# Optimization experiments

Hardware: AMD Instinct MI355X
Metric: run time of the kernel (lower is better)

The kernel has to match this reference:

```python
import jax, jax.numpy as jnp
import numpy as np

H = 16          # num heads
DH = 64         # head dim
D = H * DH      # hidden = 1024


def setup_inputs() -> dict:
    key = jax.random.key(0)
    ks = jax.random.split(key, 9)
    s = 1.0 / np.sqrt(D)
    return {
        "hidden_states": jax.random.normal(ks[0], (4, 2048, D), dtype=jnp.float32),
        "Wq": jax.random.normal(ks[1], (D, D), dtype=jnp.float32) * s,
        "bq": jax.random.normal(ks[2], (D,), dtype=jnp.float32) * 0.02,
        "Wk": jax.random.normal(ks[3], (D, D), dtype=jnp.float32) * s,
        "bk": jax.random.normal(ks[4], (D,), dtype=jnp.float32) * 0.02,
        "Wv": jax.random.normal(ks[5], (D, D), dtype=jnp.float32) * s,
        "bv": jax.random.normal(ks[6], (D,), dtype=jnp.float32) * 0.02,
        "Wo": jax.random.normal(ks[7], (D, D), dtype=jnp.float32) * s,
        "bo": jax.random.normal(ks[8], (D,), dtype=jnp.float32) * 0.02,
    }


def _split_heads(x):  # [B,S,D] -> [B,H,S,DH]
    B, S, _ = x.shape
    return x.reshape(B, S, H, DH).transpose(0, 2, 1, 3)


def reference(hidden_states, Wq, bq, Wk, bk, Wv, bv, Wo, bo):
    # torch Linear: y = x @ W.T + b  (W stored as [out, in])
    q = _split_heads(jnp.einsum('bsd,ed->bse', hidden_states, Wq) + bq)
    k = _split_heads(jnp.einsum('bsd,ed->bse', hidden_states, Wk) + bk)
    v = _split_heads(jnp.einsum('bsd,ed->bse', hidden_states, Wv) + bv)
    scores = jnp.einsum('bhqd,bhkd->bhqk', q, k) / np.sqrt(DH)
    probs = jax.nn.softmax(scores, axis=-1)  # fused softmax+matmul in original
    ctx = jnp.einsum('bhqk,bhkd->bhqd', probs, v)
    B, _, S, _ = ctx.shape
    ctx = ctx.transpose(0, 2, 1, 3).reshape(B, S, D)
    out = jnp.einsum('bsd,ed->bse', ctx, Wo) + bo
    return out  # weights are None (vis=False); dropout rate asserted 0
```

## Files before the change

kernel.cpp:

```cpp
#include <hip/hip_runtime.h>


typedef __bf16 bf16;
typedef __bf16 bf16x8 __attribute__((ext_vector_type(8)));
typedef __bf16 bf16x4 __attribute__((ext_vector_type(4)));
typedef short  short4v __attribute__((ext_vector_type(4)));
typedef float  floatx4 __attribute__((ext_vector_type(4)));

#define NB   4
#define SEQ  2048
#define NH   16
#define DH   64
#define DIM  1024
#define MTOT (NB * SEQ)

__device__ __forceinline__ floatx4 zero4() {
    floatx4 z; z[0] = 0.f; z[1] = 0.f; z[2] = 0.f; z[3] = 0.f; return z;
}

__device__ __forceinline__ void load_lds16(const bf16* g, bf16* l) {
    __builtin_amdgcn_global_load_lds(
        (__attribute__((address_space(1))) void*)g,
        (__attribute__((address_space(3))) void*)l,
        16, 0, 0);
}

__device__ __forceinline__ short4v pk4(float a, float b, float c, float d) {
    bf16x4 t; t[0] = (bf16)a; t[1] = (bf16)b; t[2] = (bf16)c; t[3] = (bf16)d;
    return __builtin_bit_cast(short4v, t);
}

__global__ __launch_bounds__(256) void cvt_kernel(const float* __restrict__ in,
                                                  bf16* __restrict__ out, int n) {
    int i = (blockIdx.x * 256 + threadIdx.x) * 4;
    if (i + 3 < n) {
        float4 f = *(const float4*)(in + i);
        bf16x4 o;
        o[0] = (bf16)f.x; o[1] = (bf16)f.y; o[2] = (bf16)f.z; o[3] = (bf16)f.w;
        *(bf16x4*)(out + i) = o;
    }
}

__global__ __launch_bounds__(256) void cvt4_kernel(const float* __restrict__ w0,
                                                   const float* __restrict__ w1,
                                                   const float* __restrict__ w2,
                                                   const float* __restrict__ w3,
                                                   bf16* __restrict__ out) {
    const float* src = (blockIdx.y == 0) ? w0 : (blockIdx.y == 1) ? w1
                     : (blockIdx.y == 2) ? w2 : w3;
    size_t i = ((size_t)blockIdx.x * 256 + threadIdx.x) * 4;
    float4 f = *(const float4*)(src + i);
    bf16x4 o;
    o[0] = (bf16)f.x; o[1] = (bf16)f.y; o[2] = (bf16)f.z; o[3] = (bf16)f.w;
    *(bf16x4*)(out + (size_t)blockIdx.y * (DIM * DIM) + i) = o;
}

__global__ __launch_bounds__(256) void gemm_qkv(const bf16* __restrict__ A,
                                                const bf16* __restrict__ W,
                                                const float* __restrict__ bq,
                                                const float* __restrict__ bk,
                                                const float* __restrict__ bv,
                                                bf16* __restrict__ Qo,
                                                bf16* __restrict__ Ko,
                                                bf16* __restrict__ Vt) {
    __shared__ __align__(16) bf16 As[128 * 32];
    __shared__ __align__(16) bf16 Bs[128 * 32];
    __shared__ __align__(16) bf16 Ts[64 * 136];

    const int tid  = threadIdx.x;
    const int wave = tid >> 6, lane = tid & 63;
    const int quad = lane >> 4, l16 = lane & 15;
    const int sel = blockIdx.x >> 3;
    const int nt  = blockIdx.x & 7;
    const int m0 = blockIdx.y * 128, n0 = nt * 128;
    const int wm = (wave & 1) * 64, wn = (wave >> 1) * 64;
    const bf16* Wsel = W + (size_t)(sel * DIM + n0) * DIM;
    const float* bias = (sel == 0) ? bq : (sel == 1) ? bk : bv;

    floatx4 acc[4][4];
#pragma unroll
    for (int mi = 0; mi < 4; mi++)
#pragma unroll
        for (int ni = 0; ni < 4; ni++) acc[mi][ni] = zero4();

    for (int k0 = 0; k0 < DIM; k0 += 32) {
        __syncthreads();
#pragma unroll
        for (int i = 0; i < 2; i++) {
            const int cb = wave * 128 + i * 64;
            const int c  = cb + lane;
            const int row = c >> 2;
            const int kc  = (c & 3) * 8;
            load_lds16(A + (size_t)(m0 + row) * DIM + k0 + kc, &As[cb * 8]);
            load_lds16(Wsel + (size_t)row * DIM + k0 + kc, &Bs[cb * 8]);
        }
        __syncthreads();

        bf16x8 af[4], bfr[4];
#pragma unroll
        for (int mi = 0; mi < 4; mi++)
            af[mi] = *(const bf16x8*)&As[(wm + mi * 16 + l16) * 32 + quad * 8];
#pragma unroll
        for (int ni = 0; ni < 4; ni++)
            bfr[ni] = *(const bf16x8*)&Bs[(wn + ni * 16 + l16) * 32 + quad * 8];
#pragma unroll
        for (int mi = 0; mi < 4; mi++)
#pragma unroll
            for (int ni = 0; ni < 4; ni++)
                acc[mi][ni] = __builtin_amdgcn_mfma_f32_16x16x32_bf16(
                    af[mi], bfr[ni], acc[mi][ni], 0, 0, 0);
    }

    if (sel < 2) {
        bf16* C = (sel == 0) ? Qo : Ko;
#pragma unroll
        for (int mi = 0; mi < 4; mi++) {
            const int rbase = m0 + wm + mi * 16 + quad * 4;
#pragma unroll
            for (int ni = 0; ni < 4; ni++) {
                const int col = n0 + wn + ni * 16 + l16;
                const float bval = bias[col];
#pragma unroll
                for (int i = 0; i < 4; i++)
                    C[(size_t)(rbase + i) * DIM + col] = (bf16)(acc[mi][ni][i] + bval);
            }
        }
    } else {
        const int b  = blockIdx.y >> 4;
        const int s0 = (blockIdx.y & 15) * 128;
#pragma unroll
        for (int r = 0; r < 2; r++) {
            __syncthreads();
            if ((wave >> 1) == r) {
#pragma unroll
                for (int mi = 0; mi < 4; mi++) {
                    const int m_l = wm + mi * 16 + quad * 4;
#pragma unroll
                    for (int ni = 0; ni < 4; ni++) {
                        const int n_loc = ni * 16 + l16;
                        const float bval = bias[n0 + 64 * r + n_loc];
#pragma unroll
                        for (int i = 0; i < 4; i++)
                            Ts[n_loc * 136 + m_l + i] = (bf16)(acc[mi][ni][i] + bval);
                    }
                }
            }
            __syncthreads();
            const int hh = 2 * nt + r;
            bf16* obase = Vt + ((size_t)(b * NH + hh) * DH) * SEQ + s0;
#pragma unroll
            for (int p = 0; p < 4; p++) {
                const int chunk = p * 256 + tid;
                const int row = chunk >> 4, c0 = (chunk & 15) * 8;
                bf16x8 v = *(const bf16x8*)&Ts[row * 136 + c0];
                *(bf16x8*)(obase + (size_t)row * SEQ + c0) = v;
            }
        }
    }
}

__global__ __launch_bounds__(256) void gemm_out(const bf16* __restrict__ A,
                                                const bf16* __restrict__ W,
                                                const float* __restrict__ bias,
                                                float* __restrict__ C) {
    __shared__ __align__(16) bf16 As[128 * 32];
    __shared__ __align__(16) bf16 Bs[128 * 32];

    const int tid  = threadIdx.x;
    const int wave = tid >> 6, lane = tid & 63;
    const int quad = lane >> 4, l16 = lane & 15;
    const int m0 = blockIdx.y * 128, n0 = blockIdx.x * 128;
    const int wm = (wave & 1) * 64, wn = (wave >> 1) * 64;

    floatx4 acc[4][4];
#pragma unroll
    for (int mi = 0; mi < 4; mi++)
#pragma unroll
        for (int ni = 0; ni < 4; ni++) acc[mi][ni] = zero4();

    for (int k0 = 0; k0 < DIM; k0 += 32) {
        __syncthreads();
#pragma unroll
        for (int i = 0; i < 2; i++) {
            const int cb = wave * 128 + i * 64;
            const int c  = cb + lane;
            const int row = c >> 2;
            const int kc  = (c & 3) * 8;
            load_lds16(A + (size_t)(m0 + row) * DIM + k0 + kc, &As[cb * 8]);
            load_lds16(W + (size_t)(n0 + row) * DIM + k0 + kc, &Bs[cb * 8]);
        }
        __syncthreads();

        bf16x8 af[4], bfr[4];
#pragma unroll
        for (int mi = 0; mi < 4; mi++)
            af[mi] = *(const bf16x8*)&As[(wm + mi * 16 + l16) * 32 + quad * 8];
#pragma unroll
        for (int ni = 0; ni < 4; ni++)
            bfr[ni] = *(const bf16x8*)&Bs[(wn + ni * 16 + l16) * 32 + quad * 8];
#pragma unroll
        for (int mi = 0; mi < 4; mi++)
#pragma unroll
            for (int ni = 0; ni < 4; ni++)
                acc[mi][ni] = __builtin_amdgcn_mfma_f32_16x16x32_bf16(
                    af[mi], bfr[ni], acc[mi][ni], 0, 0, 0);
    }

#pragma unroll
    for (int mi = 0; mi < 4; mi++) {
        const int rbase = m0 + wm + mi * 16 + quad * 4;
#pragma unroll
        for (int ni = 0; ni < 4; ni++) {
            const int col = n0 + wn + ni * 16 + l16;
            const float bval = bias[col];
#pragma unroll
            for (int i = 0; i < 4; i++)
                C[(size_t)(rbase + i) * DIM + col] = acc[mi][ni][i] + bval;
        }
    }
}

__global__ __launch_bounds__(256, 4) void attn_kernel(const bf16* __restrict__ Q,
                                                      const bf16* __restrict__ K,
                                                      const bf16* __restrict__ Vt,
                                                      bf16* __restrict__ Ctx) {
    __shared__ __align__(16) bf16 Ks[64 * 64];
    __shared__ __align__(16) bf16 Vs[64 * 64];

    const int tid  = threadIdx.x;
    const int wave = tid >> 6, lane = tid & 63;
    const int quad = lane >> 4, l16 = lane & 15;
    const int bh = blockIdx.x >> 4;
    const int qb = blockIdx.x & 15;
    const int b  = bh >> 4, h = bh & 15;

    const size_t base_bh = (size_t)b * SEQ * DIM + (size_t)h * DH;
    const size_t base_v  = (size_t)bh * DH * SEQ;
    const bf16* Kg = K + base_bh;
    const bf16* Vg = Vt + base_v;
    const int qt = qb * 128 + wave * 32;

    bf16x8 aq[2][2];
#pragma unroll
    for (int m = 0; m < 2; m++) {
        const bf16* qp = Q + base_bh + (size_t)(qt + m * 16 + l16) * DIM + quad * 8;
        aq[m][0] = *(const bf16x8*)qp;
        aq[m][1] = *(const bf16x8*)(qp + 32);
    }

    const short4v ones4 = pk4(1.f, 1.f, 1.f, 1.f);
    const float CEXP = 0.18033688f;

    floatx4 acc[2][4], accl[2];
#pragma unroll
    for (int m = 0; m < 2; m++) {
        accl[m] = zero4();
#pragma unroll
        for (int dt = 0; dt < 4; dt++) acc[m][dt] = zero4();
    }

    for (int kv0 = 0; kv0 < SEQ; kv0 += 64) {
        __syncthreads();
#pragma unroll
        for (int i = 0; i < 2; i++) {
            const int cb = wave * 128 + i * 64;
            const int c  = cb + lane;
            const int row = c >> 3;
            const int col8 = (c & 7) ^ (row & 7);
            load_lds16(Kg + (size_t)(kv0 + row) * DIM + col8 * 8, &Ks[cb * 8]);
            load_lds16(Vg + (size_t)row * SEQ + kv0 + col8 * 8, &Vs[cb * 8]);
        }
        __syncthreads();

#pragma unroll
        for (int t = 0; t < 4; t++) {
            const int krow = t * 16 + l16;
            const bf16x8 kb0 = *(const bf16x8*)&Ks[(krow * 8 + (quad ^ (krow & 7))) * 8];
            const bf16x8 kb1 = *(const bf16x8*)&Ks[(krow * 8 + ((4 + quad) ^ (krow & 7))) * 8];
            short4v vb[4];
#pragma unroll
            for (int dt = 0; dt < 4; dt++) {
                const int d = dt * 16 + l16;
                vb[dt] = __builtin_bit_cast(short4v, *(const bf16x4*)
                    &Vs[(d * 8 + ((t * 2 + (quad >> 1)) ^ (d & 7))) * 8 + (quad & 1) * 4]);
            }
#pragma unroll
            for (int m = 0; m < 2; m++) {
                floatx4 z = zero4();
                z = __builtin_amdgcn_mfma_f32_16x16x32_bf16(kb0, aq[m][0], z, 0, 0, 0);
                z = __builtin_amdgcn_mfma_f32_16x16x32_bf16(kb1, aq[m][1], z, 0, 0, 0);
                const short4v p = pk4(exp2f(z[0] * CEXP), exp2f(z[1] * CEXP),
                                      exp2f(z[2] * CEXP), exp2f(z[3] * CEXP));
#pragma unroll
                for (int dt = 0; dt < 4; dt++)
                    acc[m][dt] = __builtin_amdgcn_mfma_f32_16x16x16bf16_1k(
                        p, vb[dt], acc[m][dt], 0, 0, 0);
                accl[m] = __builtin_amdgcn_mfma_f32_16x16x16bf16_1k(
                    p, ones4, accl[m], 0, 0, 0);
            }
        }
    }

#pragma unroll
    for (int m = 0; m < 2; m++) {
        float inv[4];
#pragma unroll
        for (int i = 0; i < 4; i++) inv[i] = 1.0f / accl[m][i];
        bf16* cp = Ctx + base_bh + (size_t)(qt + m * 16 + quad * 4) * DIM + l16;
#pragma unroll
        for (int i = 0; i < 4; i++)
#pragma unroll
            for (int dt = 0; dt < 4; dt++)
                cp[(size_t)i * DIM + dt * 16] = (bf16)(acc[m][dt][i] * inv[i]);
    }
}

extern "C" void kernel_launch(void* const* d_in, const int* in_sizes, int n_in,
                              void* d_out, int out_size, void* d_ws, size_t ws_size,
                              hipStream_t stream) {
    const float* X  = (const float*)d_in[0];
    const float* Wq = (const float*)d_in[1];
    const float* bq = (const float*)d_in[2];
    const float* Wk = (const float*)d_in[3];
    const float* bk = (const float*)d_in[4];
    const float* Wv = (const float*)d_in[5];
    const float* bv = (const float*)d_in[6];
    const float* Wo = (const float*)d_in[7];
    const float* bo = (const float*)d_in[8];
    float* out = (float*)d_out;

    const size_t MD = (size_t)MTOT * DIM;
    const size_t DD = (size_t)DIM * DIM;

    bf16* Xb  = (bf16*)d_ws;
    bf16* Qb  = Xb + MD;
    bf16* Kb  = Qb + MD;
    bf16* Vtb = Kb + MD;
    bf16* Wqb = Vtb + MD;
    bf16* Wob = Wqb + 3 * DD;
    if (ws_size < (MD * 4 + DD * 4) * sizeof(bf16)) return;

    cvt_kernel<<<(int)(MD / 4 / 256), 256, 0, stream>>>(X, Xb, (int)MD);
    cvt4_kernel<<<dim3(DIM * DIM / 1024, 4), 256, 0, stream>>>(Wq, Wk, Wv, Wo, Wqb);

    gemm_qkv<<<dim3(24, MTOT / 128), 256, 0, stream>>>(Xb, Wqb, bq, bk, bv,
                                                       Qb, Kb, Vtb);

    attn_kernel<<<NB * NH * (SEQ / 128), 256, 0, stream>>>(Qb, Kb, Vtb, Xb);

    gemm_out<<<dim3(8, MTOT / 128), 256, 0, stream>>>(Xb, Wob, bo, out);
}
```

Baseline: 319.1 us.

## Fold softmax scale into Q projection and halve attention query tile per block

Pre-multiplies Q by the exp2 softmax scale in the QKV GEMM epilogue, removing a multiply per score in attention. Attention blocks now process 64 queries with 16 per wave instead of 128 with 32, doubling the grid and raising the occupancy hint to 6. This cuts registers per thread and improves latency hiding, but halves K/V tile reuse per load, doubling K/V traffic and sync overhead per FLOP.

```diff
diff --git a/kernel.cpp b/kernel.cpp
--- a/kernel.cpp
+++ b/kernel.cpp
@@ -13,6 +13,8 @@
 #define DH   64
 #define DIM  1024
 #define MTOT (NB * SEQ)
+
+#define CEXP 0.18033688f
 
 __device__ __forceinline__ floatx4 zero4() {
     floatx4 z; z[0] = 0.f; z[1] = 0.f; z[2] = 0.f; z[3] = 0.f; return z;
@@ -76,6 +78,7 @@
     const int wm = (wave & 1) * 64, wn = (wave >> 1) * 64;
     const bf16* Wsel = W + (size_t)(sel * DIM + n0) * DIM;
     const float* bias = (sel == 0) ? bq : (sel == 1) ? bk : bv;
+    const float scale = (sel == 0) ? CEXP : 1.0f;
 
     floatx4 acc[4][4];
 #pragma unroll
@@ -122,7 +125,8 @@
                 const float bval = bias[col];
 #pragma unroll
                 for (int i = 0; i < 4; i++)
-                    C[(size_t)(rbase + i) * DIM + col] = (bf16)(acc[mi][ni][i] + bval);
+                    C[(size_t)(rbase + i) * DIM + col] =
+                        (bf16)((acc[mi][ni][i] + bval) * scale);
             }
         }
     } else {
@@ -220,7 +224,7 @@
     }
 }
 
-__global__ __launch_bounds__(256, 4) void attn_kernel(const bf16* __restrict__ Q,
+__global__ __launch_bounds__(256, 6) void attn_kernel(const bf16* __restrict__ Q,
                                                       const bf16* __restrict__ K,
                                                       const bf16* __restrict__ Vt,
                                                       bf16* __restrict__ Ctx) {
@@ -230,34 +234,25 @@
     const int tid  = threadIdx.x;
     const int wave = tid >> 6, lane = tid & 63;
     const int quad = lane >> 4, l16 = lane & 15;
-    const int bh = blockIdx.x >> 4;
-    const int qb = blockIdx.x & 15;
+    const int bh = blockIdx.x >> 5;
+    const int qb = blockIdx.x & 31;
     const int b  = bh >> 4, h = bh & 15;
 
     const size_t base_bh = (size_t)b * SEQ * DIM + (size_t)h * DH;
     const size_t base_v  = (size_t)bh * DH * SEQ;
     const bf16* Kg = K + base_bh;
     const bf16* Vg = Vt + base_v;
-    const int qt = qb * 128 + wave * 32;
-
-    bf16x8 aq[2][2];
-#pragma unroll
-    for (int m = 0; m < 2; m++) {
-        const bf16* qp = Q + base_bh + (size_t)(qt + m * 16 + l16) * DIM + quad * 8;
-        aq[m][0] = *(const bf16x8*)qp;
-        aq[m][1] = *(const bf16x8*)(qp + 32);
-    }
+    const int qt = qb * 64 + wave * 16;
+
+    const bf16* qp = Q + base_bh + (size_t)(qt + l16) * DIM + quad * 8;
+    const bf16x8 aq0 = *(const bf16x8*)qp;
+    const bf16x8 aq1 = *(const bf16x8*)(qp + 32);
 
     const short4v ones4 = pk4(1.f, 1.f, 1.f, 1.f);
-    const float CEXP = 0.18033688f;
-
-    floatx4 acc[2][4], accl[2];
-#pragma unroll
-    for (int m = 0; m < 2; m++) {
-        accl[m] = zero4();
-#pragma unroll
-        for (int dt = 0; dt < 4; dt++) acc[m][dt] = zero4();
-    }
+
+    floatx4 acc[4], accl = zero4();
+#pragma unroll
+    for (int dt = 0; dt < 4; dt++) acc[dt] = zero4();
 
     for (int kv0 = 0; kv0 < SEQ; kv0 += 64) {
         __syncthreads();
@@ -284,35 +279,29 @@
                 vb[dt] = __builtin_bit_cast(short4v, *(const bf16x4*)
                     &Vs[(d * 8 + ((t * 2 + (quad >> 1)) ^ (d & 7))) * 8 + (quad & 1) * 4]);
             }
-#pragma unroll
-            for (int m = 0; m < 2; m++) {
-                floatx4 z = zero4();
-                z = __builtin_amdgcn_mfma_f32_16x16x32_bf16(kb0, aq[m][0], z, 0, 0, 0);
-                z = __builtin_amdgcn_mfma_f32_16x16x32_bf16(kb1, aq[m][1], z, 0, 0, 0);
-                const short4v p = pk4(exp2f(z[0] * CEXP), exp2f(z[1] * CEXP),
-                                      exp2f(z[2] * CEXP), exp2f(z[3] * CEXP));
-#pragma unroll
-                for (int dt = 0; dt < 4; dt++)
-                    acc[m][dt] = __builtin_amdgcn_mfma_f32_16x16x16bf16_1k(
-                        p, vb[dt], acc[m][dt], 0, 0, 0);
-                accl[m] = __builtin_amdgcn_mfma_f32_16x16x16bf16_1k(
-                    p, ones4, accl[m], 0, 0, 0);
-            }
-        }
-    }
-
-#pragma unroll
-    for (int m = 0; m < 2; m++) {
-        float inv[4];
-#pragma unroll
-        for (int i = 0; i < 4; i++) inv[i] = 1.0f / accl[m][i];
-        bf16* cp = Ctx + base_bh + (size_t)(qt + m * 16 + quad * 4) * DIM + l16;
-#pragma unroll
-        for (int i = 0; i < 4; i++)
+            floatx4 z = zero4();
+            z = __builtin_amdgcn_mfma_f32_16x16x32_bf16(kb0, aq0, z, 0, 0, 0);
+            z = __builtin_amdgcn_mfma_f32_16x16x32_bf16(kb1, aq1, z, 0, 0, 0);
+            const short4v p = pk4(exp2f(z[0]), exp2f(z[1]),
+                                  exp2f(z[2]), exp2f(z[3]));
 #pragma unroll
             for (int dt = 0; dt < 4; dt++)
-                cp[(size_t)i * DIM + dt * 16] = (bf16)(acc[m][dt][i] * inv[i]);
-    }
+                acc[dt] = __builtin_amdgcn_mfma_f32_16x16x16bf16_1k(
+                    p, vb[dt], acc[dt], 0, 0, 0);
+            accl = __builtin_amdgcn_mfma_f32_16x16x16bf16_1k(
+                p, ones4, accl, 0, 0, 0);
+        }
+    }
+
+    float inv[4];
+#pragma unroll
+    for (int i = 0; i < 4; i++) inv[i] = 1.0f / accl[i];
+    bf16* cp = Ctx + base_bh + (size_t)(qt + quad * 4) * DIM + l16;
+#pragma unroll
+    for (int i = 0; i < 4; i++)
+#pragma unroll
+        for (int dt = 0; dt < 4; dt++)
+            cp[(size_t)i * DIM + dt * 16] = (bf16)(acc[dt][i] * inv[i]);
 }
 
 extern "C" void kernel_launch(void* const* d_in, const int* in_sizes, int n_in,
@@ -346,7 +335,7 @@
     gemm_qkv<<<dim3(24, MTOT / 128), 256, 0, stream>>>(Xb, Wqb, bq, bk, bv,
                                                        Qb, Kb, Vtb);
 
-    attn_kernel<<<NB * NH * (SEQ / 128), 256, 0, stream>>>(Qb, Kb, Vtb, Xb);
+    attn_kernel<<<NB * NH * (SEQ / 64), 256, 0, stream>>>(Qb, Kb, Vtb, Xb);
 
     gemm_out<<<dim3(8, MTOT / 128), 256, 0, stream>>>(Xb, Wob, bo, out);
 }
```

New measurement: 326.3 us. 2.3% more time.
